# Kernel tuning notes

Measured on AMD Instinct MI355X. Metric: run time of the kernel, lower is better.

The kernel has to match this reference:

```python
import jax, jax.numpy as jnp
import numpy as np


def setup_inputs() -> dict:
    key = jax.random.key(0)
    k1, k2 = jax.random.split(key)
    H = W = 4096
    input1 = jax.random.normal(k1, (1, 1, H, W), dtype=jnp.float32)   # moving image
    input2 = jax.random.normal(k2, (1, 2, H, W), dtype=jnp.float32)   # dense flow (dH, dW)
    return {"input1": input1, "input2": input2}


def reference(input1, input2):
    # input1: [B=1, C=1, H, W] image; input2: [B=1, 2, H, W] displacement field
    B, C, H, W = input1.shape
    f32 = jnp.float32

    # identity mesh (matches torch.linspace outer-product construction)
    h_mesh = jnp.broadcast_to(jnp.arange(H, dtype=f32)[None, :, None], (B, H, W))
    w_mesh = jnp.broadcast_to(jnp.arange(W, dtype=f32)[None, None, :], (B, H, W))

    # warped sampling coordinates, shifted by +1 for the zero-padding border
    H_up = (input2[:, 0] + h_mesh).reshape(-1) + 1.0   # [B*H*W]
    W_up = (input2[:, 1] + w_mesh).reshape(-1) + 1.0

    # zero-pad image by 1 pixel on each spatial side
    img = jnp.pad(input1, ((0, 0), (0, 0), (1, 1), (1, 1)))  # [B, C, H+2, W+2]
    Hp, Wp = H + 2, W + 2

    hf = jnp.floor(H_up).astype(jnp.int32)
    hc = hf + 1
    wf = jnp.floor(W_up).astype(jnp.int32)
    wc = wf + 1
    hf = jnp.clip(hf, 0, Hp - 1)
    hc = jnp.clip(hc, 0, Hp - 1)
    wf = jnp.clip(wf, 0, Wp - 1)
    wc = jnp.clip(wc, 0, Wp - 1)

    img_flat = img.reshape(-1)  # B = C = 1
    val_000 = img_flat[hf * Wp + wf]
    val_010 = img_flat[hc * Wp + wf]
    val_001 = img_flat[hf * Wp + wc]
    val_011 = img_flat[hc * Wp + wc]

    dH = hc.astype(f32) - H_up
    dW = wc.astype(f32) - W_up
    out = (val_000 * (dW * dH)
           + val_010 * (dW * (1.0 - dH))
           + val_001 * ((1.0 - dW) * dH)
           + val_011 * ((1.0 - dW) * (1.0 - dH)))

    # [B*H*W] -> [B, H, W, C] -> [B, C, H, W]
    return out.reshape(B, H, W, C).transpose(0, 3, 1, 2)
```

## Files before the change

### kernel.cpp

```cpp
#include <hip/hip_runtime.h>


#define IMG_H 4096
#define IMG_W 4096
#define TR 16
#define TC 128
#define HALO 8
#define SR (TR + 2 * HALO)
#define SC (TC + 2 * HALO)
#define SC4 (SC / 4)
#define NCHUNK (SR * SC4)

typedef float f2  __attribute__((ext_vector_type(2)));
typedef float f2u __attribute__((ext_vector_type(2), aligned(4)));
typedef float f4  __attribute__((ext_vector_type(4)));

__device__ __forceinline__ float full_pixel(const float* __restrict__ img,
                                            float fhv, float fwv, int h, int w)
{
    float Hu = (fhv + (float)h) + 1.0f;
    float Wu = (fwv + (float)w) + 1.0f;

    int hf = (int)floorf(Hu);
    int wf = (int)floorf(Wu);
    int hc = hf + 1;
    int wc = wf + 1;

    int hfc = min(max(hf, 0), IMG_H + 1);
    int hcc = min(max(hc, 0), IMG_H + 1);
    int wfc = min(max(wf, 0), IMG_W + 1);
    int wcc = min(max(wc, 0), IMG_W + 1);

    float dH = (float)hcc - Hu;
    float dW = (float)wcc - Wu;

    int rf = hfc - 1, rc = hcc - 1, cf = wfc - 1, cc = wcc - 1;
    bool rf_in = (unsigned)rf < IMG_H;
    bool rc_in = (unsigned)rc < IMG_H;
    bool cf_in = (unsigned)cf < IMG_W;
    bool cc_in = (unsigned)cc < IMG_W;

    int rf_cl = min(max(rf, 0), IMG_H - 1);
    int rc_cl = min(max(rc, 0), IMG_H - 1);
    int cf_cl = min(max(cf, 0), IMG_W - 1);
    int cc_cl = min(max(cc, 0), IMG_W - 1);
    int cb    = min(max(cf, 0), IMG_W - 2);

    int sf = cf_cl - cb;
    int sc = cc_cl - cb;

    float A = dW * dH;
    float B = dW * (1.0f - dH);
    float C = (1.0f - dW) * dH;
    float D = (1.0f - dW) * (1.0f - dH);
    float w00 = (rf_in && cf_in) ? A : 0.0f;
    float w10 = (rc_in && cf_in) ? B : 0.0f;
    float w01 = (rf_in && cc_in) ? C : 0.0f;
    float w11 = (rc_in && cc_in) ? D : 0.0f;

    float a0x = (sf ? 0.0f : w00) + (sc ? 0.0f : w01);
    float a0y = (sf ? w00 : 0.0f) + (sc ? w01 : 0.0f);
    float a1x = (sf ? 0.0f : w10) + (sc ? 0.0f : w11);
    float a1y = (sf ? w10 : 0.0f) + (sc ? w11 : 0.0f);

    f2u p0 = *(const f2u*)(img + (rf_cl << 12) + cb);
    f2u p1 = *(const f2u*)(img + (rc_cl << 12) + cb);
    return p0.x * a0x + p0.y * a0y + p1.x * a1x + p1.y * a1y;
}

__global__ __launch_bounds__(256) void warp_bilinear_kernel(
    const float* __restrict__ img,
    const float* __restrict__ flow,
    float* __restrict__ out)
{
    __shared__ float tile[SR * SC];

    const int HW   = IMG_H * IMG_W;
    const int tid  = threadIdx.x;
    const int lane = tid & 63;
    const int wv   = tid >> 6;
    const int bx   = blockIdx.x, by = blockIdx.y;
    const int w0   = bx * TC + lane * 2;
    const int h0   = by * TR + wv * 4;
    const int r_lo = by * TR - HALO;
    const int c_lo = bx * TC - HALO;

    const bool border = (bx == 0) | (bx == gridDim.x - 1) |
                        (by == 0) | (by == gridDim.y - 1);

    int rowidx[4];
    f2  fh[4], fw[4];
    #pragma unroll
    for (int r = 0; r < 4; ++r)
        rowidx[r] = (h0 + r) * IMG_W + w0;
    #pragma unroll
    for (int r = 0; r < 4; ++r)
        fh[r] = __builtin_nontemporal_load((const f2*)(flow + rowidx[r]));
    #pragma unroll
    for (int r = 0; r < 4; ++r)
        fw[r] = __builtin_nontemporal_load((const f2*)(flow + HW + rowidx[r]));

    if (!border) {
        #pragma unroll
        for (int it = 0; it < 5; ++it) {
            int t = tid + it * 256;
            if (t < NCHUNK) {
                int i  = t / SC4;
                int m  = t - i * SC4;
                int gr = min(max(r_lo + i, 0), IMG_H - 1);
                int gc = min(max(c_lo + 4 * m, 0), IMG_W - 4);
                f4 v = *(const f4*)(img + gr * IMG_W + gc);
                *(f4*)(tile + i * SC + 4 * m) = v;
            }
        }
    }
    __syncthreads();

    if (border) {
        #pragma unroll
        for (int r = 0; r < 4; ++r) {
            f2 res;
            #pragma unroll
            for (int c = 0; c < 2; ++c)
                res[c] = full_pixel(img, fh[r][c], fw[r][c], h0 + r, w0 + c);
            __builtin_nontemporal_store(res, (f2*)(out + rowidx[r]));
        }
        return;
    }

    int   li0[4][2], li1[4][2];
    float A_[4][2], B_[4][2], C_[4][2], D_[4][2];
    bool  ok = true;
    const int rbase = -1 - r_lo;
    const int cbase = -1 - c_lo;

    #pragma unroll
    for (int r = 0; r < 4; ++r) {
        #pragma unroll
        for (int c = 0; c < 2; ++c) {
            float Hu = (fh[r][c] + (float)(h0 + r)) + 1.0f;
            float Wu = (fw[r][c] + (float)(w0 + c)) + 1.0f;

            int hf = (int)floorf(Hu);
            int wf = (int)floorf(Wu);
            float dH = (float)(hf + 1) - Hu;
            float dW = (float)(wf + 1) - Wu;

            int i0 = hf + rbase;
            int jb = wf + cbase;
            ok = ok && ((unsigned)i0 < SR - 1) && ((unsigned)jb < SC - 1);
            li0[r][c] = i0 * SC + jb;
            li1[r][c] = li0[r][c] + SC;

            float omH = 1.0f - dH, omW = 1.0f - dW;
            A_[r][c] = dW * dH;
            C_[r][c] = omW * dH;
            B_[r][c] = dW * omH;
            D_[r][c] = omW * omH;
        }
    }

    float res[4][2];
    if (__builtin_expect(ok, 1)) {
        float q0x[4][2], q0y[4][2], q1x[4][2], q1y[4][2];
        #pragma unroll
        for (int r = 0; r < 4; ++r)
            #pragma unroll
            for (int c = 0; c < 2; ++c) {
                q0x[r][c] = tile[li0[r][c]];
                q0y[r][c] = tile[li0[r][c] + 1];
                q1x[r][c] = tile[li1[r][c]];
                q1y[r][c] = tile[li1[r][c] + 1];
            }
        #pragma unroll
        for (int r = 0; r < 4; ++r)
            #pragma unroll
            for (int c = 0; c < 2; ++c)
                res[r][c] = q0x[r][c] * A_[r][c] + q0y[r][c] * C_[r][c]
                          + q1x[r][c] * B_[r][c] + q1y[r][c] * D_[r][c];
    }
    if (__builtin_expect(!ok, 0)) {
        #pragma unroll
        for (int r = 0; r < 4; ++r)
            #pragma unroll
            for (int c = 0; c < 2; ++c)
                res[r][c] = full_pixel(img, fh[r][c], fw[r][c],
                                       h0 + r, w0 + c);
    }

    #pragma unroll
    for (int r = 0; r < 4; ++r) {
        f2 v; v[0] = res[r][0]; v[1] = res[r][1];
        __builtin_nontemporal_store(v, (f2*)(out + rowidx[r]));
    }
}

extern "C" void kernel_launch(void* const* d_in, const int* in_sizes, int n_in,
                              void* d_out, int out_size, void* d_ws, size_t ws_size,
                              hipStream_t stream) {
    const float* img  = (const float*)d_in[0];
    const float* flow = (const float*)d_in[1];
    float* out = (float*)d_out;

    dim3 grid(IMG_W / TC, IMG_H / TR);
    dim3 block(256);
    warp_bilinear_kernel<<<grid, block, 0, stream>>>(img, flow, out);
}
```

Measured before the change: 254.8 us.

## Process four row tiles per block with double-buffered LDS staging

Each block now handles four vertically stacked 16x128 tiles in sequence. It double-buffers the shared-memory image tile and the flow registers, so the next tile's global loads are issued before the current tile is computed. This amortizes per-block setup and index computation and overlaps memory latency with compute. The cost is a quarter as many blocks, which may hurt occupancy and load balance, plus more registers and twice the LDS. Border handling is now done per tile rather than per block.

```diff
diff --git a/kernel.cpp b/kernel.cpp
--- a/kernel.cpp
+++ b/kernel.cpp
@@ -10,6 +10,9 @@
 #define SC (TC + 2 * HALO)
 #define SC4 (SC / 4)
 #define NCHUNK (SR * SC4)
+#define KT 4
+#define BTR (TR * KT)
+#define NTY (IMG_H / TR)
 
 typedef float f2  __attribute__((ext_vector_type(2)));
 typedef float f2u __attribute__((ext_vector_type(2), aligned(4)));
@@ -73,7 +76,7 @@
     const float* __restrict__ flow,
     float* __restrict__ out)
 {
-    __shared__ float tile[SR * SC];
+    __shared__ float tile[2][SR * SC];
 
     const int HW   = IMG_H * IMG_W;
     const int tid  = threadIdx.x;
@@ -81,117 +84,171 @@
     const int wv   = tid >> 6;
     const int bx   = blockIdx.x, by = blockIdx.y;
     const int w0   = bx * TC + lane * 2;
-    const int h0   = by * TR + wv * 4;
-    const int r_lo = by * TR - HALO;
     const int c_lo = bx * TC - HALO;
 
-    const bool border = (bx == 0) | (bx == gridDim.x - 1) |
-                        (by == 0) | (by == gridDim.y - 1);
-
-    int rowidx[4];
-    f2  fh[4], fw[4];
-    #pragma unroll
-    for (int r = 0; r < 4; ++r)
-        rowidx[r] = (h0 + r) * IMG_W + w0;
-    #pragma unroll
-    for (int r = 0; r < 4; ++r)
-        fh[r] = __builtin_nontemporal_load((const f2*)(flow + rowidx[r]));
-    #pragma unroll
-    for (int r = 0; r < 4; ++r)
-        fw[r] = __builtin_nontemporal_load((const f2*)(flow + HW + rowidx[r]));
-
-    if (!border) {
-        #pragma unroll
-        for (int it = 0; it < 5; ++it) {
-            int t = tid + it * 256;
-            if (t < NCHUNK) {
-                int i  = t / SC4;
-                int m  = t - i * SC4;
-                int gr = min(max(r_lo + i, 0), IMG_H - 1);
-                int gc = min(max(c_lo + 4 * m, 0), IMG_W - 4);
-                f4 v = *(const f4*)(img + gr * IMG_W + gc);
-                *(f4*)(tile + i * SC + 4 * m) = v;
-            }
-        }
-    }
-    __syncthreads();
-
-    if (border) {
-        #pragma unroll
-        for (int r = 0; r < 4; ++r) {
-            f2 res;
-            #pragma unroll
-            for (int c = 0; c < 2; ++c)
-                res[c] = full_pixel(img, fh[r][c], fw[r][c], h0 + r, w0 + c);
-            __builtin_nontemporal_store(res, (f2*)(out + rowidx[r]));
+    if (bx == 0 || bx == (int)gridDim.x - 1) {
+        #pragma unroll
+        for (int t = 0; t < KT; ++t) {
+            const int h0 = by * BTR + t * TR + wv * 4;
+            int rowidx[4]; f2 fh[4], fw[4];
+            #pragma unroll
+            for (int r = 0; r < 4; ++r)
+                rowidx[r] = (h0 + r) * IMG_W + w0;
+            #pragma unroll
+            for (int r = 0; r < 4; ++r)
+                fh[r] = __builtin_nontemporal_load((const f2*)(flow + rowidx[r]));
+            #pragma unroll
+            for (int r = 0; r < 4; ++r)
+                fw[r] = __builtin_nontemporal_load((const f2*)(flow + HW + rowidx[r]));
+            #pragma unroll
+            for (int r = 0; r < 4; ++r) {
+                f2 res;
+                #pragma unroll
+                for (int c = 0; c < 2; ++c)
+                    res[c] = full_pixel(img, fh[r][c], fw[r][c], h0 + r, w0 + c);
+                __builtin_nontemporal_store(res, (f2*)(out + rowidx[r]));
+            }
         }
         return;
     }
 
-    int   li0[4][2], li1[4][2];
-    float A_[4][2], B_[4][2], C_[4][2], D_[4][2];
-    bool  ok = true;
-    const int rbase = -1 - r_lo;
-    const int cbase = -1 - c_lo;
-
+    int  sg_i[5], sg_m[5];
+    bool sg_on[5];
     #pragma unroll
-    for (int r = 0; r < 4; ++r) {
-        #pragma unroll
-        for (int c = 0; c < 2; ++c) {
-            float Hu = (fh[r][c] + (float)(h0 + r)) + 1.0f;
-            float Wu = (fw[r][c] + (float)(w0 + c)) + 1.0f;
-
-            int hf = (int)floorf(Hu);
-            int wf = (int)floorf(Wu);
-            float dH = (float)(hf + 1) - Hu;
-            float dW = (float)(wf + 1) - Wu;
-
-            int i0 = hf + rbase;
-            int jb = wf + cbase;
-            ok = ok && ((unsigned)i0 < SR - 1) && ((unsigned)jb < SC - 1);
-            li0[r][c] = i0 * SC + jb;
-            li1[r][c] = li0[r][c] + SC;
-
-            float omH = 1.0f - dH, omW = 1.0f - dW;
-            A_[r][c] = dW * dH;
-            C_[r][c] = omW * dH;
-            B_[r][c] = dW * omH;
-            D_[r][c] = omW * omH;
+    for (int it = 0; it < 5; ++it) {
+        int t = tid + it * 256;
+        sg_on[it] = (t < NCHUNK);
+        sg_i[it]  = t / SC4;
+        sg_m[it]  = (t - sg_i[it] * SC4) * 4;
+    }
+
+    const int  ty0  = by * KT;
+    const bool tb_f = (ty0 == 0);
+    const bool tb_l = (ty0 + KT - 1 == NTY - 1);
+
+    auto stage = [&](int buf, int t) {
+        const int r_lo = by * BTR + t * TR - HALO;
+        #pragma unroll
+        for (int it = 0; it < 5; ++it)
+            if (sg_on[it]) {
+                f4 v = *(const f4*)(img + (r_lo + sg_i[it]) * IMG_W
+                                       + (c_lo + sg_m[it]));
+                *(f4*)(&tile[buf][sg_i[it] * SC + sg_m[it]]) = v;
+            }
+    };
+
+    f2  FH[2][4], FW[2][4];
+    int RI[2][4];
+    auto flowload = [&](int buf, int t) {
+        const int h0 = by * BTR + t * TR + wv * 4;
+        #pragma unroll
+        for (int r = 0; r < 4; ++r)
+            RI[buf][r] = (h0 + r) * IMG_W + w0;
+        #pragma unroll
+        for (int r = 0; r < 4; ++r)
+            FH[buf][r] = __builtin_nontemporal_load((const f2*)(flow + RI[buf][r]));
+        #pragma unroll
+        for (int r = 0; r < 4; ++r)
+            FW[buf][r] = __builtin_nontemporal_load((const f2*)(flow + HW + RI[buf][r]));
+    };
+
+    if (!tb_f) stage(0, 0);
+    flowload(0, 0);
+    __syncthreads();
+
+    #pragma unroll
+    for (int t = 0; t < KT; ++t) {
+        const int cur = t & 1;
+
+        if (t + 1 < KT) {
+            const bool nb = (t + 1 == KT - 1) && tb_l;
+            if (!nb) stage(cur ^ 1, t + 1);
+            flowload(cur ^ 1, t + 1);
         }
-    }
-
-    float res[4][2];
-    if (__builtin_expect(ok, 1)) {
-        float q0x[4][2], q0y[4][2], q1x[4][2], q1y[4][2];
-        #pragma unroll
-        for (int r = 0; r < 4; ++r)
-            #pragma unroll
-            for (int c = 0; c < 2; ++c) {
-                q0x[r][c] = tile[li0[r][c]];
-                q0y[r][c] = tile[li0[r][c] + 1];
-                q1x[r][c] = tile[li1[r][c]];
-                q1y[r][c] = tile[li1[r][c] + 1];
-            }
-        #pragma unroll
-        for (int r = 0; r < 4; ++r)
-            #pragma unroll
-            for (int c = 0; c < 2; ++c)
-                res[r][c] = q0x[r][c] * A_[r][c] + q0y[r][c] * C_[r][c]
-                          + q1x[r][c] * B_[r][c] + q1y[r][c] * D_[r][c];
-    }
-    if (__builtin_expect(!ok, 0)) {
-        #pragma unroll
-        for (int r = 0; r < 4; ++r)
-            #pragma unroll
-            for (int c = 0; c < 2; ++c)
-                res[r][c] = full_pixel(img, fh[r][c], fw[r][c],
-                                       h0 + r, w0 + c);
-    }
-
-    #pragma unroll
-    for (int r = 0; r < 4; ++r) {
-        f2 v; v[0] = res[r][0]; v[1] = res[r][1];
-        __builtin_nontemporal_store(v, (f2*)(out + rowidx[r]));
+
+        const bool thisb = (t == 0 && tb_f) || (t == KT - 1 && tb_l);
+        const int  h0    = by * BTR + t * TR + wv * 4;
+
+        if (thisb) {
+            #pragma unroll
+            for (int r = 0; r < 4; ++r) {
+                f2 res;
+                #pragma unroll
+                for (int c = 0; c < 2; ++c)
+                    res[c] = full_pixel(img, FH[cur][r][c], FW[cur][r][c],
+                                        h0 + r, w0 + c);
+                __builtin_nontemporal_store(res, (f2*)(out + RI[cur][r]));
+            }
+        } else {
+            const int r_lo  = by * BTR + t * TR - HALO;
+            const int rbase = -1 - r_lo;
+            const int cbase = -1 - c_lo;
+
+            int   li0[4][2];
+            float A_[4][2], B_[4][2], C_[4][2], D_[4][2];
+            bool  ok = true;
+
+            #pragma unroll
+            for (int r = 0; r < 4; ++r) {
+                #pragma unroll
+                for (int c = 0; c < 2; ++c) {
+                    float Hu = (FH[cur][r][c] + (float)(h0 + r)) + 1.0f;
+                    float Wu = (FW[cur][r][c] + (float)(w0 + c)) + 1.0f;
+
+                    int hf = (int)floorf(Hu);
+                    int wf = (int)floorf(Wu);
+                    float dH = (float)(hf + 1) - Hu;
+                    float dW = (float)(wf + 1) - Wu;
+
+                    int i0 = hf + rbase;
+                    int jb = wf + cbase;
+                    ok = ok && ((unsigned)i0 < SR - 1) && ((unsigned)jb < SC - 1);
+                    li0[r][c] = i0 * SC + jb;
+
+                    float omH = 1.0f - dH, omW = 1.0f - dW;
+                    A_[r][c] = dW * dH;
+                    C_[r][c] = omW * dH;
+                    B_[r][c] = dW * omH;
+                    D_[r][c] = omW * omH;
+                }
+            }
+
+            float res[4][2];
+            if (__builtin_expect(ok, 1)) {
+                float q0x[4][2], q0y[4][2], q1x[4][2], q1y[4][2];
+                #pragma unroll
+                for (int r = 0; r < 4; ++r)
+                    #pragma unroll
+                    for (int c = 0; c < 2; ++c) {
+                        q0x[r][c] = tile[cur][li0[r][c]];
+                        q0y[r][c] = tile[cur][li0[r][c] + 1];
+                        q1x[r][c] = tile[cur][li0[r][c] + SC];
+                        q1y[r][c] = tile[cur][li0[r][c] + SC + 1];
+                    }
+                #pragma unroll
+                for (int r = 0; r < 4; ++r)
+                    #pragma unroll
+                    for (int c = 0; c < 2; ++c)
+                        res[r][c] = q0x[r][c] * A_[r][c] + q0y[r][c] * C_[r][c]
+                                  + q1x[r][c] * B_[r][c] + q1y[r][c] * D_[r][c];
+            }
+            if (__builtin_expect(!ok, 0)) {
+                #pragma unroll
+                for (int r = 0; r < 4; ++r)
+                    #pragma unroll
+                    for (int c = 0; c < 2; ++c)
+                        res[r][c] = full_pixel(img, FH[cur][r][c], FW[cur][r][c],
+                                               h0 + r, w0 + c);
+            }
+
+            #pragma unroll
+            for (int r = 0; r < 4; ++r) {
+                f2 v; v[0] = res[r][0]; v[1] = res[r][1];
+                __builtin_nontemporal_store(v, (f2*)(out + RI[cur][r]));
+            }
+        }
+
+        if (t + 1 < KT) __syncthreads();
     }
 }
 
@@ -202,7 +259,7 @@
     const float* flow = (const float*)d_in[1];
     float* out = (float*)d_out;
 
-    dim3 grid(IMG_W / TC, IMG_H / TR);
+    dim3 grid(IMG_W / TC, IMG_H / BTR);
     dim3 block(256);
     warp_bilinear_kernel<<<grid, block, 0, stream>>>(img, flow, out);
 }
```

After: 260.6 us. +2.3%, slower.
